# Optimization experiments

Hardware: AMD Instinct MI355X
Metric: run time of the kernel (lower is better)

The kernel has to match this reference:

```python
import jax, jax.numpy as jnp
import numpy as np

N_SERIES = 4096
MAX_STEP = 2
NUM_MATS = 2 * MAX_STEP + 1  # len(supports)*K + 1


def setup_inputs() -> dict:
    key = jax.random.key(0)
    ks = jax.random.split(key, 6)
    B, N, C, D, O = 4, N_SERIES, 2, 64, 64
    F = C + D  # 66
    scale = 1.0 / jnp.sqrt(jnp.float32(N))  # keep diffusion powers numerically sane
    xavier = jnp.sqrt(2.0 / (F * NUM_MATS + O)).astype(jnp.float32)
    return {
        "inputs": jax.random.normal(ks[0], (B, N * C), dtype=jnp.float32),
        "state": jax.random.normal(ks[1], (B, N * D), dtype=jnp.float32),
        "support0": jax.random.normal(ks[2], (N, N), dtype=jnp.float32) * scale,
        "support1": jax.random.normal(ks[3], (N, N), dtype=jnp.float32) * scale,
        "weight": jax.random.normal(ks[4], (F * NUM_MATS, O), dtype=jnp.float32) * xavier,
        "biases": jnp.zeros((O,), dtype=jnp.float32),
        "output_size": 64,
    }


def reference(inputs, state, support0, support1, weight, biases, output_size):
    B = inputs.shape[0]
    N = N_SERIES
    x_in = inputs.reshape(B, N, -1)
    h_in = state.reshape(B, N, -1)
    xs = jnp.concatenate([x_in, h_in], axis=2)  # [B, N, F]
    F = xs.shape[2]
    # (N, F, B) -> (N, F*B), matching torch permute(1,2,0).reshape
    x0 = jnp.transpose(xs, (1, 2, 0)).reshape(N, F * B)
    mats = [x0]
    # Faithful to source: x0 is mutated inside the loop and carries over
    # between supports (the Chebyshev recurrence quirk of the original).
    for support in (support0, support1):
        x1 = support @ x0
        mats.append(x1)
        for _ in range(2, MAX_STEP + 1):
            x2 = 2.0 * (support @ x1) - x0
            mats.append(x2)
            x1, x0 = x2, x1
    x = jnp.stack(mats, axis=0)  # [num_mats, N, F*B]
    x = x.reshape(NUM_MATS, N, F, B)
    x = jnp.transpose(x, (3, 1, 2, 0))  # [B, N, F, num_mats]
    x = x.reshape(B * N, F * NUM_MATS)
    out = x @ weight + biases  # [B*N, O]
    return out.reshape(B, N * output_size)
```

## Files before the change

### kernel.cpp

```cpp
#include <hip/hip_runtime.h>
#include <stdint.h>

typedef unsigned short u16;
typedef u16 u16x4 __attribute__((ext_vector_type(4)));
typedef u16 u16x8 __attribute__((ext_vector_type(8)));
typedef __bf16 bf16x8 __attribute__((ext_vector_type(8)));
typedef float f32x4 __attribute__((ext_vector_type(4)));

#define NSER 4096
#define KDIM 4096
#define NCOLS 288
#define MATSZ (NCOLS * NSER)
#define PE ((size_t)NCOLS * NSER)

__device__ __forceinline__ u16 f2bf(float f) {
  uint32_t u = __builtin_bit_cast(uint32_t, f);
  u += 0x7FFFu + ((u >> 16) & 1u);
  return (u16)(u >> 16);
}
__device__ __forceinline__ float bf2f(u16 h) {
  return __builtin_bit_cast(float, (uint32_t)h << 16);
}

typedef const void __attribute__((address_space(1)))* gas1p;
typedef void __attribute__((address_space(3)))* las3p;

__device__ __forceinline__ void gload16(const void* g, void* l) {
  __builtin_amdgcn_global_load_lds((gas1p)g, (las3p)l, 16, 0, 0);
}

__global__ __launch_bounds__(256) void k_build_x(const float* __restrict__ inputs,
                                                 const float* __restrict__ state,
                                                 u16* __restrict__ xb) {
  __shared__ float tile[64][65];
  const int nt = blockIdx.x, b = blockIdx.y;
  const int n0 = nt * 64;
  const int t = threadIdx.x;
  {
    const int i = t >> 2;
    const int c0 = (t & 3) * 16;
    const float* sp = state + ((int64_t)b * NSER + (n0 + i)) * 64 + c0;
    #pragma unroll
    for (int q = 0; q < 4; ++q) {
      float4 v = *(const float4*)(sp + q * 4);
      tile[i][c0 + q * 4 + 0] = v.x;
      tile[i][c0 + q * 4 + 1] = v.y;
      tile[i][c0 + q * 4 + 2] = v.z;
      tile[i][c0 + q * 4 + 3] = v.w;
    }
  }
  __syncthreads();
  const int wv = t >> 6, lane = t & 63;
  #pragma unroll
  for (int it = 0; it < 16; ++it) {
    const int d = wv + 4 * it;
    xb[(size_t)((2 + d) * 4 + b) * NSER + n0 + lane] = f2bf(tile[lane][d]);
  }
  if (t < 128) {
    const int c = t >> 6, j = t & 63;
    xb[(size_t)(c * 4 + b) * NSER + n0 + j] =
        f2bf(inputs[(int64_t)b * (NSER * 2) + (int64_t)(n0 + j) * 2 + c]);
  }
  if (b == 0) {
    for (int idx = t; idx < 24 * 64; idx += 256)
      xb[(size_t)(264 + idx / 64) * NSER + n0 + (idx & 63)] = 0;
  }
}

#define BM 64
#define BN 96
#define BK 64
#define KC 4
#define ABYTES (BM * BK * 2)
#define BBYTES (BN * BK * 2)
#define BUFSZ  (ABYTES + BBYTES)

__global__ __launch_bounds__(256) void k_gemm(const float* __restrict__ A0f,
                                              const float* __restrict__ A1f,
                                              const u16* __restrict__ Bm,
                                              float* __restrict__ Pb) {
  int kc = blockIdx.z;
  const float* Af = A0f;
  if (kc >= KC) { Af = A1f; kc -= KC; }
  const int i0 = blockIdx.x * BM;
  const int j0 = blockIdx.y * BN;
  const int t = threadIdx.x;
  const int wid = t >> 6, lane = t & 63;
  const int NKT = KDIM / KC / BK;
  const int k0 = kc * (KDIM / KC);

  __shared__ char smem[2 * BUFSZ];

  int a_grow[2], a_ldst[2];
  #pragma unroll
  for (int s = 0; s < 2; ++s) {
    const int row = (wid * 2 + s) * 8 + (lane >> 3);
    a_grow[s] = row * KDIM + (lane & 7) * 8;
    a_ldst[s] = row * 128 + 16 * ((lane & 7) ^ (row & 7));
  }
  int b_src[3];
  #pragma unroll
  for (int s = 0; s < 3; ++s) {
    const int row = (wid * 3 + s) * 8 + (lane >> 3);
    b_src[s] = row * (KDIM * 2) + 16 * ((lane & 7) ^ (row & 7));
  }
  const float* Ag = Af + (int64_t)i0 * KDIM + k0;
  const char* Bg = (const char*)Bm + ((int64_t)j0 * KDIM + k0) * 2;

  int aoffs[2], axors[2];
  #pragma unroll
  for (int mf = 0; mf < 2; ++mf) {
    const int row = (wid >> 1) * 32 + mf * 16 + (lane & 15);
    aoffs[mf] = row * 128;
    axors[mf] = (row & 7) << 4;
  }
  int boffs[3], bxors[3];
  #pragma unroll
  for (int nf = 0; nf < 3; ++nf) {
    const int row = (wid & 1) * 48 + nf * 16 + (lane & 15);
    boffs[nf] = ABYTES + row * 128;
    bxors[nf] = (row & 7) << 4;
  }
  const int klane = (lane >> 4) * 16;

  f32x4 acc[2][3];
  #pragma unroll
  for (int mf = 0; mf < 2; ++mf)
    #pragma unroll
    for (int nf = 0; nf < 3; ++nf)
      acc[mf][nf] = (f32x4){0.f, 0.f, 0.f, 0.f};

  f32x4 areg[2][2];

  #pragma unroll
  for (int s = 0; s < 2; ++s) {
    areg[s][0] = *(const f32x4*)(Ag + a_grow[s]);
    areg[s][1] = *(const f32x4*)(Ag + a_grow[s] + 4);
  }
  #pragma unroll
  for (int s = 0; s < 3; ++s)
    gload16(Bg + b_src[s], smem + ABYTES + (wid * 3 + s) * 1024);
  #pragma unroll
  for (int s = 0; s < 2; ++s) {
    u16x8 w;
    #pragma unroll
    for (int q = 0; q < 4; ++q) { w[q] = f2bf(areg[s][0][q]); w[4 + q] = f2bf(areg[s][1][q]); }
    *(u16x8*)(smem + a_ldst[s]) = w;
  }
  __syncthreads();

  for (int kt = 0; kt < NKT; ++kt) {
    const int cur = kt & 1;
    char* sbuf = smem + (cur ^ 1) * BUFSZ;
    if (kt + 1 < NKT) {
      const float* Ak = Ag + (kt + 1) * BK;
      const char* Bk = Bg + (kt + 1) * (BK * 2);
      #pragma unroll
      for (int s = 0; s < 2; ++s) {
        areg[s][0] = *(const f32x4*)(Ak + a_grow[s]);
        areg[s][1] = *(const f32x4*)(Ak + a_grow[s] + 4);
      }
      #pragma unroll
      for (int s = 0; s < 3; ++s)
        gload16(Bk + b_src[s], sbuf + ABYTES + (wid * 3 + s) * 1024);
    }
    const char* sb = smem + cur * BUFSZ;
    #pragma unroll
    for (int kk = 0; kk < 2; ++kk) {
      const int kb = kk * 64 + klane;
      bf16x8 af[2], bfv[3];
      #pragma unroll
      for (int mf = 0; mf < 2; ++mf)
        af[mf] = *(const bf16x8*)(sb + aoffs[mf] + (kb ^ axors[mf]));
      #pragma unroll
      for (int nf = 0; nf < 3; ++nf)
        bfv[nf] = *(const bf16x8*)(sb + boffs[nf] + (kb ^ bxors[nf]));
      #pragma unroll
      for (int mf = 0; mf < 2; ++mf)
        #pragma unroll
        for (int nf = 0; nf < 3; ++nf)
          acc[mf][nf] = __builtin_amdgcn_mfma_f32_16x16x32_bf16(af[mf], bfv[nf],
                                                                acc[mf][nf], 0, 0, 0);
    }
    if (kt + 1 < NKT) {
      #pragma unroll
      for (int s = 0; s < 2; ++s) {
        u16x8 w;
        #pragma unroll
        for (int q = 0; q < 4; ++q) { w[q] = f2bf(areg[s][0][q]); w[4 + q] = f2bf(areg[s][1][q]); }
        *(u16x8*)(sbuf + a_ldst[s]) = w;
      }
    }
    __syncthreads();
  }

  float* Pp = Pb + (size_t)blockIdx.z * PE;
  #pragma unroll
  for (int mf = 0; mf < 2; ++mf) {
    const int i = i0 + (wid >> 1) * 32 + mf * 16 + ((lane >> 4) << 2);
    #pragma unroll
    for (int nf = 0; nf < 3; ++nf) {
      const int j = j0 + (wid & 1) * 48 + nf * 16 + (lane & 15);
      *(f32x4*)(Pp + (size_t)j * NSER + i) = acc[mf][nf];
    }
  }
}

__global__ __launch_bounds__(256) void k_reduce(const float* __restrict__ P,
                                                u16* __restrict__ o) {
  const size_t i = ((size_t)blockIdx.x * 256 + threadIdx.x) * 4;
  f32x4 s = *(const f32x4*)(P + i);
  #pragma unroll
  for (int k = 1; k < 4; ++k)
    s += *(const f32x4*)(P + (size_t)k * PE + i);
  u16x4 w;
  #pragma unroll
  for (int r = 0; r < 4; ++r) w[r] = f2bf(s[r]);
  *(u16x4*)(o + i) = w;
}

__global__ __launch_bounds__(256) void k_final(const float* __restrict__ weight,
                                               const float* __restrict__ biases,
                                               const u16* __restrict__ Xb,
                                               const u16* __restrict__ m1b,
                                               const u16* __restrict__ m3b,
                                               const float* __restrict__ P,
                                               float* __restrict__ out) {
  __shared__ float w2[330][32];
  const int nt = blockIdx.x, b = blockIdx.y, oh = blockIdx.z;
  const int n0 = nt * 64;
  const int t = threadIdx.x;
  const int lane = t & 63, wv = t >> 6;
  {
    const int ol = t & 31;
    const int o = oh * 32 + ol;
    for (int f = t >> 5; f < 66; f += 8) {
      const float v0 = weight[(f * 5 + 0) * 64 + o];
      const float v1 = weight[(f * 5 + 1) * 64 + o];
      const float v2 = weight[(f * 5 + 2) * 64 + o];
      const float v3 = weight[(f * 5 + 3) * 64 + o];
      const float v4 = weight[(f * 5 + 4) * 64 + o];
      w2[f * 5 + 0][ol] = v0 - v2;
      w2[f * 5 + 1][ol] = v1 - v4;
      w2[f * 5 + 2][ol] = 2.f * v2;
      w2[f * 5 + 3][ol] = v3;
      w2[f * 5 + 4][ol] = 2.f * v4;
    }
  }
  __syncthreads();
  const int ob = oh * 32 + wv * 8;
  float acc[8];
  #pragma unroll
  for (int i = 0; i < 8; ++i) acc[i] = biases[ob + i];
  for (int f = 0; f < 66; ++f) {
    const size_t base = (size_t)(f * 4 + b) * NSER + n0 + lane;
    float y[5];
    y[0] = bf2f(Xb[base]);
    y[1] = bf2f(m1b[base]);
    y[2] = P[base] + P[PE + base] + P[2 * PE + base] + P[3 * PE + base];
    y[3] = bf2f(m3b[base]);
    y[4] = P[4 * PE + base] + P[5 * PE + base] + P[6 * PE + base] + P[7 * PE + base];
    #pragma unroll
    for (int mat = 0; mat < 5; ++mat) {
      const float* wr = &w2[f * 5 + mat][wv * 8];
      #pragma unroll
      for (int i = 0; i < 8; ++i) acc[i] = fmaf(y[mat], wr[i], acc[i]);
    }
  }
  float* op = out + (size_t)b * (NSER * 64) + (size_t)(n0 + lane) * 64 + ob;
  #pragma unroll
  for (int i = 0; i < 8; ++i) op[i] = acc[i];
}

extern "C" void kernel_launch(void* const* d_in, const int* in_sizes, int n_in,
                              void* d_out, int out_size, void* d_ws, size_t ws_size,
                              hipStream_t stream) {
  const float* inputs = (const float*)d_in[0];
  const float* state  = (const float*)d_in[1];
  const float* s0     = (const float*)d_in[2];
  const float* s1     = (const float*)d_in[3];
  const float* weight = (const float*)d_in[4];
  const float* biases = (const float*)d_in[5];
  float* out = (float*)d_out;

  char* ws = (char*)d_ws;
  u16* Xb  = (u16*)ws;
  u16* m1b = Xb + MATSZ;
  u16* m3b = m1b + MATSZ;
  float* P = (float*)(ws + (size_t)3 * 2359296);

  k_build_x<<<dim3(64, 4, 1), 256, 0, stream>>>(inputs, state, Xb);
  k_gemm<<<dim3(64, 3, 4), 256, 0, stream>>>(s0, s0, Xb, P);
  k_reduce<<<dim3(1152, 1, 1), 256, 0, stream>>>(P, m1b);
  k_gemm<<<dim3(64, 3, 8), 256, 0, stream>>>(s0, s1, m1b, P);
  k_reduce<<<dim3(1152, 1, 1), 256, 0, stream>>>(P + 4 * PE, m3b);
  k_gemm<<<dim3(64, 3, 4), 256, 0, stream>>>(s1, s1, m3b, P + 4 * PE);
  k_final<<<dim3(64, 4, 2), 256, 0, stream>>>(weight, biases, Xb, m1b, m3b, P, out);
}
```

Measured before the change: 140.4 us.

## Triple-buffer LDS to prefetch B tiles two k-steps ahead

Grows shared memory from two to three tile buffers and rotates them so the B-tile global-to-LDS loads run two iterations ahead, while the fp32 A loads stay one iteration ahead. __syncthreads is replaced with an explicit lgkmcnt wait plus s_barrier wrapped in sched_barriers, so outstanding B loads are no longer drained at every barrier. This aims to hide global memory latency better. In exchange it uses more LDS per block, which may lower occupancy, and it relies on in-order vmcnt behaviour for the LDS-DMA loads to be correct.

```diff
diff --git a/kernel.cpp b/kernel.cpp
--- a/kernel.cpp
+++ b/kernel.cpp
@@ -89,7 +89,7 @@
   const int NKT = KDIM / KC / BK;
   const int k0 = kc * (KDIM / KC);
 
-  __shared__ char smem[2 * BUFSZ];
+  __shared__ char smem[3 * BUFSZ];
 
   int a_grow[2], a_ldst[2];
   #pragma unroll
@@ -133,38 +133,49 @@
   f32x4 areg[2][2];
 
   #pragma unroll
+  for (int s = 0; s < 3; ++s)
+    gload16(Bg + b_src[s], smem + ABYTES + (wid * 3 + s) * 1024);
+  #pragma unroll
   for (int s = 0; s < 2; ++s) {
     areg[s][0] = *(const f32x4*)(Ag + a_grow[s]);
     areg[s][1] = *(const f32x4*)(Ag + a_grow[s] + 4);
   }
   #pragma unroll
-  for (int s = 0; s < 3; ++s)
-    gload16(Bg + b_src[s], smem + ABYTES + (wid * 3 + s) * 1024);
-  #pragma unroll
   for (int s = 0; s < 2; ++s) {
     u16x8 w;
     #pragma unroll
     for (int q = 0; q < 4; ++q) { w[q] = f2bf(areg[s][0][q]); w[4 + q] = f2bf(areg[s][1][q]); }
     *(u16x8*)(smem + a_ldst[s]) = w;
   }
-  __syncthreads();
+  #pragma unroll
+  for (int s = 0; s < 3; ++s)
+    gload16(Bg + BK * 2 + b_src[s], smem + BUFSZ + ABYTES + (wid * 3 + s) * 1024);
+  __builtin_amdgcn_sched_barrier(0);
+  asm volatile("s_waitcnt lgkmcnt(0)");
+  __builtin_amdgcn_sched_barrier(0);
+  __builtin_amdgcn_s_barrier();
+  __builtin_amdgcn_sched_barrier(0);
+
+  int o0 = 0, o1 = BUFSZ, o2 = 2 * BUFSZ;
 
   for (int kt = 0; kt < NKT; ++kt) {
-    const int cur = kt & 1;
-    char* sbuf = smem + (cur ^ 1) * BUFSZ;
     if (kt + 1 < NKT) {
       const float* Ak = Ag + (kt + 1) * BK;
-      const char* Bk = Bg + (kt + 1) * (BK * 2);
       #pragma unroll
       for (int s = 0; s < 2; ++s) {
         areg[s][0] = *(const f32x4*)(Ak + a_grow[s]);
         areg[s][1] = *(const f32x4*)(Ak + a_grow[s] + 4);
       }
+    }
+    if (kt + 2 < NKT) {
+      const char* Bk = Bg + (kt + 2) * (BK * 2);
+      char* sb2 = smem + o2;
       #pragma unroll
       for (int s = 0; s < 3; ++s)
-        gload16(Bk + b_src[s], sbuf + ABYTES + (wid * 3 + s) * 1024);
-    }
-    const char* sb = smem + cur * BUFSZ;
+        gload16(Bk + b_src[s], sb2 + ABYTES + (wid * 3 + s) * 1024);
+    }
+    __builtin_amdgcn_sched_barrier(0);
+    const char* sb = smem + o0;
     #pragma unroll
     for (int kk = 0; kk < 2; ++kk) {
       const int kb = kk * 64 + klane;
@@ -182,16 +193,23 @@
           acc[mf][nf] = __builtin_amdgcn_mfma_f32_16x16x32_bf16(af[mf], bfv[nf],
                                                                 acc[mf][nf], 0, 0, 0);
     }
+    __builtin_amdgcn_sched_barrier(0);
     if (kt + 1 < NKT) {
+      char* sbw = smem + o1;
       #pragma unroll
       for (int s = 0; s < 2; ++s) {
         u16x8 w;
         #pragma unroll
         for (int q = 0; q < 4; ++q) { w[q] = f2bf(areg[s][0][q]); w[4 + q] = f2bf(areg[s][1][q]); }
-        *(u16x8*)(sbuf + a_ldst[s]) = w;
+        *(u16x8*)(sbw + a_ldst[s]) = w;
       }
-    }
-    __syncthreads();
+      __builtin_amdgcn_sched_barrier(0);
+      asm volatile("s_waitcnt lgkmcnt(0)");
+      __builtin_amdgcn_sched_barrier(0);
+      __builtin_amdgcn_s_barrier();
+      __builtin_amdgcn_sched_barrier(0);
+    }
+    const int tmp = o0; o0 = o1; o1 = o2; o2 = tmp;
   }
 
   float* Pp = Pb + (size_t)blockIdx.z * PE;
```

After: 159.3 us. 13.5% more time.

## Write back bf16 copies of supports during first GEMM and reuse them later

Applied to the files above, without the earlier changes.

The first GEMM pass over each fp32 support matrix now also writes a bf16 copy into workspace, and later GEMMs load that copy with direct-to-LDS loads instead of re-reading and converting fp32. This is meant to halve the bytes read for the support matrices in the second and third GEMMs and to skip repeated conversion work. The first GEMM also moves to an 8-way K split, which gives more blocks and adds reduction traffic. Which path runs depends on the workspace size, so the gain only appears when enough scratch space is provided.

```diff
diff --git a/kernel.cpp b/kernel.cpp
--- a/kernel.cpp
+++ b/kernel.cpp
@@ -70,33 +70,43 @@
 #define BM 64
 #define BN 96
 #define BK 64
-#define KC 4
 #define ABYTES (BM * BK * 2)
 #define BBYTES (BN * BK * 2)
 #define BUFSZ  (ABYTES + BBYTES)
 
-__global__ __launch_bounds__(256) void k_gemm(const float* __restrict__ A0f,
-                                              const float* __restrict__ A1f,
+template <int KCC, int M0, int M1>
+__global__ __launch_bounds__(256) void k_gemm(const float* __restrict__ Af0,
+                                              const float* __restrict__ Af1,
+                                              const u16* __restrict__ Ab0,
+                                              const u16* __restrict__ Ab1,
+                                              u16* __restrict__ wb0,
+                                              u16* __restrict__ wb1,
                                               const u16* __restrict__ Bm,
                                               float* __restrict__ Pb) {
   int kc = blockIdx.z;
-  const float* Af = A0f;
-  if (kc >= KC) { Af = A1f; kc -= KC; }
+  int unit = 0;
+  if (kc >= KCC) { unit = 1; kc -= KCC; }
+  const int mode = unit ? M1 : M0;
+  const float* Af = unit ? Af1 : Af0;
+  const u16* Ab = unit ? Ab1 : Ab0;
+  u16* wb = unit ? wb1 : wb0;
   const int i0 = blockIdx.x * BM;
   const int j0 = blockIdx.y * BN;
   const int t = threadIdx.x;
   const int wid = t >> 6, lane = t & 63;
-  const int NKT = KDIM / KC / BK;
-  const int k0 = kc * (KDIM / KC);
+  const int NKT = KDIM / KCC / BK;
+  const int k0 = kc * (KDIM / KCC);
+  const bool do_wb = (mode == 0) && (wb != nullptr) && (blockIdx.y == 0);
 
   __shared__ char smem[2 * BUFSZ];
 
-  int a_grow[2], a_ldst[2];
+  int a_row[2], a_grow[2], a_ldst[2], a_srcb[2];
   #pragma unroll
   for (int s = 0; s < 2; ++s) {
-    const int row = (wid * 2 + s) * 8 + (lane >> 3);
-    a_grow[s] = row * KDIM + (lane & 7) * 8;
-    a_ldst[s] = row * 128 + 16 * ((lane & 7) ^ (row & 7));
+    a_row[s] = (wid * 2 + s) * 8 + (lane >> 3);
+    a_grow[s] = a_row[s] * KDIM + (lane & 7) * 8;
+    a_ldst[s] = a_row[s] * 128 + 16 * ((lane & 7) ^ (a_row[s] & 7));
+    a_srcb[s] = a_row[s] * (KDIM * 2) + 16 * ((lane & 7) ^ (a_row[s] & 7));
   }
   int b_src[3];
   #pragma unroll
@@ -104,7 +114,9 @@
     const int row = (wid * 3 + s) * 8 + (lane >> 3);
     b_src[s] = row * (KDIM * 2) + 16 * ((lane & 7) ^ (row & 7));
   }
-  const float* Ag = Af + (int64_t)i0 * KDIM + k0;
+  const float* Agf = Af ? Af + (int64_t)i0 * KDIM + k0 : nullptr;
+  const char* Agb = Ab ? (const char*)Ab + ((int64_t)i0 * KDIM + k0) * 2 : nullptr;
+  u16* wbp = do_wb ? wb + (size_t)i0 * KDIM + k0 : nullptr;
   const char* Bg = (const char*)Bm + ((int64_t)j0 * KDIM + k0) * 2;
 
   int aoffs[2], axors[2];
@@ -133,19 +145,26 @@
   f32x4 areg[2][2];
 
   #pragma unroll
-  for (int s = 0; s < 2; ++s) {
-    areg[s][0] = *(const f32x4*)(Ag + a_grow[s]);
-    areg[s][1] = *(const f32x4*)(Ag + a_grow[s] + 4);
-  }
-  #pragma unroll
   for (int s = 0; s < 3; ++s)
     gload16(Bg + b_src[s], smem + ABYTES + (wid * 3 + s) * 1024);
-  #pragma unroll
-  for (int s = 0; s < 2; ++s) {
-    u16x8 w;
-    #pragma unroll
-    for (int q = 0; q < 4; ++q) { w[q] = f2bf(areg[s][0][q]); w[4 + q] = f2bf(areg[s][1][q]); }
-    *(u16x8*)(smem + a_ldst[s]) = w;
+  if (mode == 1) {
+    #pragma unroll
+    for (int s = 0; s < 2; ++s)
+      gload16(Agb + a_srcb[s], smem + (wid * 2 + s) * 1024);
+  } else {
+    #pragma unroll
+    for (int s = 0; s < 2; ++s) {
+      areg[s][0] = *(const f32x4*)(Agf + a_grow[s]);
+      areg[s][1] = *(const f32x4*)(Agf + a_grow[s] + 4);
+    }
+    #pragma unroll
+    for (int s = 0; s < 2; ++s) {
+      u16x8 w;
+      #pragma unroll
+      for (int q = 0; q < 4; ++q) { w[q] = f2bf(areg[s][0][q]); w[4 + q] = f2bf(areg[s][1][q]); }
+      *(u16x8*)(smem + a_ldst[s]) = w;
+      if (do_wb) *(u16x8*)(wbp + a_grow[s]) = w;
+    }
   }
   __syncthreads();
 
@@ -153,16 +172,24 @@
     const int cur = kt & 1;
     char* sbuf = smem + (cur ^ 1) * BUFSZ;
     if (kt + 1 < NKT) {
-      const float* Ak = Ag + (kt + 1) * BK;
+      if (mode == 0) {
+        const float* Ak = Agf + (kt + 1) * BK;
+        #pragma unroll
+        for (int s = 0; s < 2; ++s) {
+          areg[s][0] = *(const f32x4*)(Ak + a_grow[s]);
+          areg[s][1] = *(const f32x4*)(Ak + a_grow[s] + 4);
+        }
+      }
       const char* Bk = Bg + (kt + 1) * (BK * 2);
-      #pragma unroll
-      for (int s = 0; s < 2; ++s) {
-        areg[s][0] = *(const f32x4*)(Ak + a_grow[s]);
-        areg[s][1] = *(const f32x4*)(Ak + a_grow[s] + 4);
-      }
       #pragma unroll
       for (int s = 0; s < 3; ++s)
         gload16(Bk + b_src[s], sbuf + ABYTES + (wid * 3 + s) * 1024);
+      if (mode == 1) {
+        const char* Ak = Agb + (kt + 1) * (BK * 2);
+        #pragma unroll
+        for (int s = 0; s < 2; ++s)
+          gload16(Ak + a_srcb[s], sbuf + (wid * 2 + s) * 1024);
+      }
     }
     const char* sb = smem + cur * BUFSZ;
     #pragma unroll
@@ -182,13 +209,14 @@
           acc[mf][nf] = __builtin_amdgcn_mfma_f32_16x16x32_bf16(af[mf], bfv[nf],
                                                                 acc[mf][nf], 0, 0, 0);
     }
-    if (kt + 1 < NKT) {
+    if (mode == 0 && kt + 1 < NKT) {
       #pragma unroll
       for (int s = 0; s < 2; ++s) {
         u16x8 w;
         #pragma unroll
         for (int q = 0; q < 4; ++q) { w[q] = f2bf(areg[s][0][q]); w[4 + q] = f2bf(areg[s][1][q]); }
         *(u16x8*)(sbuf + a_ldst[s]) = w;
+        if (do_wb) *(u16x8*)(wbp + (kt + 1) * BK + a_grow[s]) = w;
       }
     }
     __syncthreads();
@@ -206,12 +234,13 @@
   }
 }
 
+template <int NS>
 __global__ __launch_bounds__(256) void k_reduce(const float* __restrict__ P,
                                                 u16* __restrict__ o) {
   const size_t i = ((size_t)blockIdx.x * 256 + threadIdx.x) * 4;
   f32x4 s = *(const f32x4*)(P + i);
   #pragma unroll
-  for (int k = 1; k < 4; ++k)
+  for (int k = 1; k < NS; ++k)
     s += *(const f32x4*)(P + (size_t)k * PE + i);
   u16x4 w;
   #pragma unroll
@@ -287,13 +316,49 @@
   u16* Xb  = (u16*)ws;
   u16* m1b = Xb + MATSZ;
   u16* m3b = m1b + MATSZ;
-  float* P = (float*)(ws + (size_t)3 * 2359296);
+
+  const size_t SB = 33554432;
+  const size_t PB = 8ull * 4718592;
+  const size_t NEED_BIG = 7077888 + 2 * SB + PB;
+  const size_t NEED_MID = 7077888 + SB + PB;
 
   k_build_x<<<dim3(64, 4, 1), 256, 0, stream>>>(inputs, state, Xb);
-  k_gemm<<<dim3(64, 3, 4), 256, 0, stream>>>(s0, s0, Xb, P);
-  k_reduce<<<dim3(1152, 1, 1), 256, 0, stream>>>(P, m1b);
-  k_gemm<<<dim3(64, 3, 8), 256, 0, stream>>>(s0, s1, m1b, P);
-  k_reduce<<<dim3(1152, 1, 1), 256, 0, stream>>>(P + 4 * PE, m3b);
-  k_gemm<<<dim3(64, 3, 4), 256, 0, stream>>>(s1, s1, m3b, P + 4 * PE);
-  k_final<<<dim3(64, 4, 2), 256, 0, stream>>>(weight, biases, Xb, m1b, m3b, P, out);
-}
+
+  if (ws_size >= NEED_BIG) {
+    u16* S0b = (u16*)(ws + 7077888);
+    u16* S1b = S0b + (SB / 2);
+    float* P = (float*)(ws + 7077888 + 2 * SB);
+    k_gemm<8, 0, 0><<<dim3(64, 3, 8), 256, 0, stream>>>(s0, s0, nullptr, nullptr,
+                                                        S0b, S0b, Xb, P);
+    k_reduce<8><<<dim3(1152, 1, 1), 256, 0, stream>>>(P, m1b);
+    k_gemm<4, 1, 0><<<dim3(64, 3, 8), 256, 0, stream>>>(nullptr, s1, S0b, nullptr,
+                                                        nullptr, S1b, m1b, P);
+    k_reduce<4><<<dim3(1152, 1, 1), 256, 0, stream>>>(P + 4 * PE, m3b);
+    k_gemm<4, 1, 1><<<dim3(64, 3, 4), 256, 0, stream>>>(nullptr, nullptr, S1b, S1b,
+                                                        nullptr, nullptr, m3b, P + 4 * PE);
+    k_final<<<dim3(64, 4, 2), 256, 0, stream>>>(weight, biases, Xb, m1b, m3b, P, out);
+  } else if (ws_size >= NEED_MID) {
+    u16* S1b = (u16*)(ws + 7077888);
+    float* P = (float*)(ws + 7077888 + SB);
+    k_gemm<8, 0, 0><<<dim3(64, 3, 8), 256, 0, stream>>>(s0, s0, nullptr, nullptr,
+                                                        nullptr, nullptr, Xb, P);
+    k_reduce<8><<<dim3(1152, 1, 1), 256, 0, stream>>>(P, m1b);
+    k_gemm<4, 0, 0><<<dim3(64, 3, 8), 256, 0, stream>>>(s0, s1, nullptr, nullptr,
+                                                        nullptr, S1b, m1b, P);
+    k_reduce<4><<<dim3(1152, 1, 1), 256, 0, stream>>>(P + 4 * PE, m3b);
+    k_gemm<4, 1, 1><<<dim3(64, 3, 4), 256, 0, stream>>>(nullptr, nullptr, S1b, S1b,
+                                                        nullptr, nullptr, m3b, P + 4 * PE);
+    k_final<<<dim3(64, 4, 2), 256, 0, stream>>>(weight, biases, Xb, m1b, m3b, P, out);
+  } else {
+    float* P = (float*)(ws + 7077888);
+    k_gemm<8, 0, 0><<<dim3(64, 3, 8), 256, 0, stream>>>(s0, s0, nullptr, nullptr,
+                                                        nullptr, nullptr, Xb, P);
+    k_reduce<8><<<dim3(1152, 1, 1), 256, 0, stream>>>(P, m1b);
+    k_gemm<4, 0, 0><<<dim3(64, 3, 8), 256, 0, stream>>>(s0, s1, nullptr, nullptr,
+                                                        nullptr, nullptr, m1b, P);
+    k_reduce<4><<<dim3(1152, 1, 1), 256, 0, stream>>>(P + 4 * PE, m3b);
+    k_gemm<4, 0, 0><<<dim3(64, 3, 4), 256, 0, stream>>>(s1, s1, nullptr, nullptr,
+                                                        nullptr, nullptr, m3b, P + 4 * PE);
+    k_final<<<dim3(64, 4, 2), 256, 0, stream>>>(weight, biases, Xb, m1b, m3b, P, out);
+  }
+}
```

New measurement: 156.6 us. 1.11x slower.

## Fuse dual-support GEMM into one block sharing B tile across two A operands

Applied to the files above, without the earlier changes.

Adds k_gemm2, which runs the s0 and s1 products against the same m1b in a single 512-thread block: four waves handle each support, and the shared B tile is loaded into LDS once by the first group. This replaces the earlier launch with 8 z-slices, halving B global and LDS traffic for that stage. The trade-off is larger LDS use and 512-thread blocks, which may reduce occupancy. The output partial layout (unit*KC+kc) matches the previous z indexing.

```diff
diff --git a/kernel.cpp b/kernel.cpp
--- a/kernel.cpp
+++ b/kernel.cpp
@@ -154,12 +154,12 @@
     char* sbuf = smem + (cur ^ 1) * BUFSZ;
     if (kt + 1 < NKT) {
       const float* Ak = Ag + (kt + 1) * BK;
-      const char* Bk = Bg + (kt + 1) * (BK * 2);
       #pragma unroll
       for (int s = 0; s < 2; ++s) {
         areg[s][0] = *(const f32x4*)(Ak + a_grow[s]);
         areg[s][1] = *(const f32x4*)(Ak + a_grow[s] + 4);
       }
+      const char* Bk = Bg + (kt + 1) * (BK * 2);
       #pragma unroll
       for (int s = 0; s < 3; ++s)
         gload16(Bk + b_src[s], sbuf + ABYTES + (wid * 3 + s) * 1024);
@@ -201,6 +201,144 @@
     #pragma unroll
     for (int nf = 0; nf < 3; ++nf) {
       const int j = j0 + (wid & 1) * 48 + nf * 16 + (lane & 15);
+      *(f32x4*)(Pp + (size_t)j * NSER + i) = acc[mf][nf];
+    }
+  }
+}
+
+#define F_BOFF (2 * ABYTES)
+#define F_BUF  (F_BOFF + BBYTES)
+
+__global__ __launch_bounds__(512) void k_gemm2(const float* __restrict__ A0f,
+                                               const float* __restrict__ A1f,
+                                               const u16* __restrict__ Bm,
+                                               float* __restrict__ Pb) {
+  const int kc = blockIdx.z;
+  const int i0 = blockIdx.x * BM;
+  const int j0 = blockIdx.y * BN;
+  const int t = threadIdx.x;
+  const int wid = t >> 6, lane = t & 63;
+  const int unit = wid >> 2, wl = wid & 3;
+  const float* Af = unit ? A1f : A0f;
+  const int NKT = KDIM / KC / BK;
+  const int k0 = kc * (KDIM / KC);
+
+  __shared__ char smem[2 * F_BUF];
+
+  int a_grow[2], a_ldst[2];
+  #pragma unroll
+  for (int s = 0; s < 2; ++s) {
+    const int row = (wl * 2 + s) * 8 + (lane >> 3);
+    a_grow[s] = row * KDIM + (lane & 7) * 8;
+    a_ldst[s] = unit * ABYTES + row * 128 + 16 * ((lane & 7) ^ (row & 7));
+  }
+  int b_src[3];
+  #pragma unroll
+  for (int s = 0; s < 3; ++s) {
+    const int row = (wl * 3 + s) * 8 + (lane >> 3);
+    b_src[s] = row * (KDIM * 2) + 16 * ((lane & 7) ^ (row & 7));
+  }
+  const float* Ag = Af + (int64_t)i0 * KDIM + k0;
+  const char* Bg = (const char*)Bm + ((int64_t)j0 * KDIM + k0) * 2;
+
+  int aoffs[2], axors[2];
+  #pragma unroll
+  for (int mf = 0; mf < 2; ++mf) {
+    const int row = (wl >> 1) * 32 + mf * 16 + (lane & 15);
+    aoffs[mf] = unit * ABYTES + row * 128;
+    axors[mf] = (row & 7) << 4;
+  }
+  int boffs[3], bxors[3];
+  #pragma unroll
+  for (int nf = 0; nf < 3; ++nf) {
+    const int row = (wl & 1) * 48 + nf * 16 + (lane & 15);
+    boffs[nf] = F_BOFF + row * 128;
+    bxors[nf] = (row & 7) << 4;
+  }
+  const int klane = (lane >> 4) * 16;
+
+  f32x4 acc[2][3];
+  #pragma unroll
+  for (int mf = 0; mf < 2; ++mf)
+    #pragma unroll
+    for (int nf = 0; nf < 3; ++nf)
+      acc[mf][nf] = (f32x4){0.f, 0.f, 0.f, 0.f};
+
+  f32x4 areg[2][2];
+
+  #pragma unroll
+  for (int s = 0; s < 2; ++s) {
+    areg[s][0] = *(const f32x4*)(Ag + a_grow[s]);
+    areg[s][1] = *(const f32x4*)(Ag + a_grow[s] + 4);
+  }
+  if (unit == 0) {
+    #pragma unroll
+    for (int s = 0; s < 3; ++s)
+      gload16(Bg + b_src[s], smem + F_BOFF + (wl * 3 + s) * 1024);
+  }
+  #pragma unroll
+  for (int s = 0; s < 2; ++s) {
+    u16x8 w;
+    #pragma unroll
+    for (int q = 0; q < 4; ++q) { w[q] = f2bf(areg[s][0][q]); w[4 + q] = f2bf(areg[s][1][q]); }
+    *(u16x8*)(smem + a_ldst[s]) = w;
+  }
+  __syncthreads();
+
+  for (int kt = 0; kt < NKT; ++kt) {
+    const int cur = kt & 1;
+    char* sbuf = smem + (cur ^ 1) * F_BUF;
+    if (kt + 1 < NKT) {
+      const float* Ak = Ag + (kt + 1) * BK;
+      #pragma unroll
+      for (int s = 0; s < 2; ++s) {
+        areg[s][0] = *(const f32x4*)(Ak + a_grow[s]);
+        areg[s][1] = *(const f32x4*)(Ak + a_grow[s] + 4);
+      }
+      if (unit == 0) {
+        const char* Bk = Bg + (kt + 1) * (BK * 2);
+        #pragma unroll
+        for (int s = 0; s < 3; ++s)
+          gload16(Bk + b_src[s], sbuf + F_BOFF + (wl * 3 + s) * 1024);
+      }
+    }
+    const char* sb = smem + cur * F_BUF;
+    #pragma unroll
+    for (int kk = 0; kk < 2; ++kk) {
+      const int kb = kk * 64 + klane;
+      bf16x8 af[2], bfv[3];
+      #pragma unroll
+      for (int mf = 0; mf < 2; ++mf)
+        af[mf] = *(const bf16x8*)(sb + aoffs[mf] + (kb ^ axors[mf]));
+      #pragma unroll
+      for (int nf = 0; nf < 3; ++nf)
+        bfv[nf] = *(const bf16x8*)(sb + boffs[nf] + (kb ^ bxors[nf]));
+      #pragma unroll
+      for (int mf = 0; mf < 2; ++mf)
+        #pragma unroll
+        for (int nf = 0; nf < 3; ++nf)
+          acc[mf][nf] = __builtin_amdgcn_mfma_f32_16x16x32_bf16(af[mf], bfv[nf],
+                                                                acc[mf][nf], 0, 0, 0);
+    }
+    if (kt + 1 < NKT) {
+      #pragma unroll
+      for (int s = 0; s < 2; ++s) {
+        u16x8 w;
+        #pragma unroll
+        for (int q = 0; q < 4; ++q) { w[q] = f2bf(areg[s][0][q]); w[4 + q] = f2bf(areg[s][1][q]); }
+        *(u16x8*)(sbuf + a_ldst[s]) = w;
+      }
+    }
+    __syncthreads();
+  }
+
+  float* Pp = Pb + (size_t)(unit * KC + kc) * PE;
+  #pragma unroll
+  for (int mf = 0; mf < 2; ++mf) {
+    const int i = i0 + (wl >> 1) * 32 + mf * 16 + ((lane >> 4) << 2);
+    #pragma unroll
+    for (int nf = 0; nf < 3; ++nf) {
+      const int j = j0 + (wl & 1) * 48 + nf * 16 + (lane & 15);
       *(f32x4*)(Pp + (size_t)j * NSER + i) = acc[mf][nf];
     }
   }
@@ -292,7 +430,7 @@
   k_build_x<<<dim3(64, 4, 1), 256, 0, stream>>>(inputs, state, Xb);
   k_gemm<<<dim3(64, 3, 4), 256, 0, stream>>>(s0, s0, Xb, P);
   k_reduce<<<dim3(1152, 1, 1), 256, 0, stream>>>(P, m1b);
-  k_gemm<<<dim3(64, 3, 8), 256, 0, stream>>>(s0, s1, m1b, P);
+  k_gemm2<<<dim3(64, 3, 4), 512, 0, stream>>>(s0, s1, m1b, P);
   k_reduce<<<dim3(1152, 1, 1), 256, 0, stream>>>(P + 4 * PE, m3b);
   k_gemm<<<dim3(64, 3, 4), 256, 0, stream>>>(s1, s1, m3b, P + 4 * PE);
   k_final<<<dim3(64, 4, 2), 256, 0, stream>>>(weight, biases, Xb, m1b, m3b, P, out);
```

New measurement: 141.4 us. Within noise of the previous version (+0.7%).
